# Kernel tuning notes

Hardware: AMD Instinct MI355X
Metric: run time of the kernel (lower is better)

Reference implementation:

```python
import jax, jax.numpy as jnp
import numpy as np

B, L, D, H = 2, 2048, 1024, 16
DH = D // H            # head depth = 64
LEN_CONTEXT = 2048 + 1 # module stores len_context + 1


def setup_inputs() -> dict:
    key = jax.random.key(0)
    ks = jax.random.split(key, 9)
    s = 0.02
    return {
        "query": jax.random.normal(ks[0], (B, L, D), jnp.float32),
        "key":   jax.random.normal(ks[1], (B, L, D), jnp.float32),
        "value": jax.random.normal(ks[2], (B, L, D), jnp.float32),
        "Wq": jax.random.normal(ks[3], (D, D), jnp.float32) * s,
        "bq": jnp.zeros((D,), jnp.float32),
        "Wk": jax.random.normal(ks[4], (D, D), jnp.float32) * s,
        "bk": jnp.zeros((D,), jnp.float32),
        "Wv": jax.random.normal(ks[5], (D, D), jnp.float32) * s,
        "bv": jnp.zeros((D,), jnp.float32),
        "Wo": jax.random.normal(ks[6], (D, D), jnp.float32) * s,
        "bo": jnp.zeros((D,), jnp.float32),
        "rel": jax.random.normal(ks[7], (LEN_CONTEXT, DH), jnp.float32) * s,
    }


def _split_heads(x):
    # [B, L, D] -> [B, H, L, DH]
    return x.reshape(B, L, H, DH).transpose(0, 2, 1, 3)


def reference(query, key, value, Wq, bq, Wk, bk, Wv, bv, Wo, bo, rel):
    q = _split_heads(query @ Wq + bq)   # [B,H,L,DH]
    k = _split_heads(key @ Wk + bk)
    v = _split_heads(value @ Wv + bv)

    # relative embedding slice: rel[max(0, len_context - len_q):]
    start = max(0, LEN_CONTEXT - L)
    e = rel[start:, :]                  # [M, DH], M = L here
    M = e.shape[0]

    qe = jnp.einsum('bhld,md->bhlm', q, e)  # [B,H,L,M]

    # _qe_masking: keep qe[l, m] where m >= M-1-l (upper anti-triangle)
    mask = (jnp.arange(M)[None, :] >= (M - 1 - jnp.arange(L))[:, None]).astype(qe.dtype)
    qe = qe * mask

    # _skewing: pad 1 on left of last dim, reshape swapping last two dims, drop first row
    padded = jnp.pad(qe, ((0, 0), (0, 0), (0, 0), (1, 0)))        # [B,H,L,M+1]
    reshaped = padded.reshape(B, H, M + 1, L)
    srel = reshaped[:, :, 1:, :]                                  # [B,H,L,L] (len_k == len_q)

    logits = (jnp.einsum('bhld,bhmd->bhlm', q, k) + srel) / jnp.sqrt(jnp.float32(DH))
    # NOTE: the original code builds a directional mask but never adds it to logits
    attn = jax.nn.softmax(logits, axis=-1)
    out = jnp.einsum('bhlm,bhmd->bhld', attn, v)                  # [B,H,L,DH]
    out = out.transpose(0, 2, 1, 3).reshape(B, L, D)
    return out @ Wo + bo
```

## Files before the change

### kernel.cpp

```cpp
#include <hip/hip_runtime.h>
#include <hip/hip_bf16.h>


typedef __bf16 v8bf __attribute__((ext_vector_type(8)));
typedef __bf16 v4bf __attribute__((ext_vector_type(4)));
typedef float f32x4 __attribute__((ext_vector_type(4)));
typedef float f32x16 __attribute__((ext_vector_type(16)));

#define MFMA16(A,B,C) __builtin_amdgcn_mfma_f32_16x16x32_bf16((A),(B),(C),0,0,0)
#define MFMA32(A,B,C) __builtin_amdgcn_mfma_f32_32x32x16_bf16((A),(B),(C),0,0,0)

__global__ __launch_bounds__(256)
void cast_rel(const float* __restrict__ rel, __bf16* __restrict__ E)
{
    const int i = blockIdx.x * 256 + threadIdx.x;
    if (i >= 2304 * 16) return;
    const int base = i * 4;
    const int row = base >> 6;
    const int prow = row - 128;
    v4bf o;
    if (prow >= 0 && prow < 2048) {
        const float4 v = *reinterpret_cast<const float4*>(&rel[(size_t)(prow + 1) * 64 + (base & 63)]);
        o[0] = (__bf16)v.x; o[1] = (__bf16)v.y; o[2] = (__bf16)v.z; o[3] = (__bf16)v.w;
    } else {
        o[0] = (__bf16)0.f; o[1] = (__bf16)0.f; o[2] = (__bf16)0.f; o[3] = (__bf16)0.f;
    }
    *reinterpret_cast<v4bf*>(&E[base]) = o;
}

__global__ __launch_bounds__(256)
void transpose_cast_w4(const float* __restrict__ W0, const float* __restrict__ W1,
                       const float* __restrict__ W2, const float* __restrict__ W3,
                       __bf16* __restrict__ Wt4)
{
    __shared__ float tile[64][65];
    const int z = blockIdx.z;
    const float* W = (z == 0) ? W0 : (z == 1) ? W1 : (z == 2) ? W2 : W3;
    __bf16* Wt = Wt4 + (size_t)z * 1048576;
    const int r0 = blockIdx.y * 64, c0 = blockIdx.x * 64;
    const int tr = threadIdx.x >> 4;
    const int tc = (threadIdx.x & 15) * 4;
    #pragma unroll
    for (int p = 0; p < 4; ++p) {
        const int r = tr + p * 16;
        const float4 v = *reinterpret_cast<const float4*>(&W[(size_t)(r0 + r) * 1024 + c0 + tc]);
        tile[r][tc + 0] = v.x; tile[r][tc + 1] = v.y; tile[r][tc + 2] = v.z; tile[r][tc + 3] = v.w;
    }
    __syncthreads();
    #pragma unroll
    for (int p = 0; p < 4; ++p) {
        const int cr = tr + p * 16;
        v4bf o;
        o[0] = (__bf16)tile[tc + 0][cr];
        o[1] = (__bf16)tile[tc + 1][cr];
        o[2] = (__bf16)tile[tc + 2][cr];
        o[3] = (__bf16)tile[tc + 3][cr];
        *reinterpret_cast<v4bf*>(&Wt[(size_t)(c0 + cr) * 1024 + r0 + tc]) = o;
    }
}

template <bool ABF16>
__device__ __forceinline__
void gemm_body(const float* __restrict__ Af, const __bf16* __restrict__ Ab,
               const __bf16* __restrict__ Wt, const float* __restrict__ bias,
               float* __restrict__ Cf, __bf16* __restrict__ Cb, int mode,
               int bx, int by)
{
    __shared__ __bf16 As[2][128 * 64];
    __shared__ __bf16 Ws[2][64 * 64];
    const int tid = threadIdx.x;
    const int wid = tid >> 6, lane = tid & 63, g = lane >> 4, li = lane & 15;
    const int r0 = by * 128, c0 = bx * 64;
    const int wr = wid >> 1, wc = wid & 1;
    const int sr = tid >> 3, sb = tid & 7;

    f32x4 acc[4][2];
    #pragma unroll
    for (int a = 0; a < 4; ++a)
        #pragma unroll
        for (int b2 = 0; b2 < 2; ++b2) acc[a][b2] = f32x4{0.f, 0.f, 0.f, 0.f};

    v8bf areg[4], wreg[2];

    auto loadA = [&](int p, int kt) -> v8bf {
        if constexpr (ABF16) {
            return *reinterpret_cast<const v8bf*>(&Ab[(size_t)(r0 + sr + 32 * p) * 1024 + kt + sb * 8]);
        } else {
            const float* ar = &Af[(size_t)(r0 + sr + 32 * p) * 1024 + kt + sb * 8];
            const float4 f0 = *reinterpret_cast<const float4*>(ar);
            const float4 f1 = *reinterpret_cast<const float4*>(ar + 4);
            v8bf a8;
            a8[0] = (__bf16)f0.x; a8[1] = (__bf16)f0.y; a8[2] = (__bf16)f0.z; a8[3] = (__bf16)f0.w;
            a8[4] = (__bf16)f1.x; a8[5] = (__bf16)f1.y; a8[6] = (__bf16)f1.z; a8[7] = (__bf16)f1.w;
            return a8;
        }
    };

    #pragma unroll
    for (int p = 0; p < 4; ++p) areg[p] = loadA(p, 0);
    #pragma unroll
    for (int p = 0; p < 2; ++p)
        wreg[p] = *reinterpret_cast<const v8bf*>(&Wt[(size_t)(c0 + sr + 32 * p) * 1024 + sb * 8]);
    #pragma unroll
    for (int p = 0; p < 4; ++p) {
        const int row = sr + 32 * p;
        *reinterpret_cast<v8bf*>(&As[0][row * 64 + ((sb ^ (row & 7)) << 3)]) = areg[p];
    }
    #pragma unroll
    for (int p = 0; p < 2; ++p) {
        const int row = sr + 32 * p;
        *reinterpret_cast<v8bf*>(&Ws[0][row * 64 + ((sb ^ (row & 7)) << 3)]) = wreg[p];
    }
    __syncthreads();

    for (int ki = 0; ki < 16; ++ki) {
        const int cur = ki & 1;
        if (ki < 15) {
            const int kt = (ki + 1) * 64;
            #pragma unroll
            for (int p = 0; p < 4; ++p) areg[p] = loadA(p, kt);
            #pragma unroll
            for (int p = 0; p < 2; ++p)
                wreg[p] = *reinterpret_cast<const v8bf*>(&Wt[(size_t)(c0 + sr + 32 * p) * 1024 + kt + sb * 8]);
        }
        #pragma unroll
        for (int ks = 0; ks < 2; ++ks) {
            v8bf af[4], bfr[2];
            #pragma unroll
            for (int fm = 0; fm < 4; ++fm) {
                const int row = wr * 64 + fm * 16 + li;
                af[fm] = *reinterpret_cast<const v8bf*>(
                    &As[cur][row * 64 + (((ks * 4 + g) ^ (row & 7)) << 3)]);
            }
            #pragma unroll
            for (int fn = 0; fn < 2; ++fn) {
                const int row = wc * 32 + fn * 16 + li;
                bfr[fn] = *reinterpret_cast<const v8bf*>(
                    &Ws[cur][row * 64 + (((ks * 4 + g) ^ (row & 7)) << 3)]);
            }
            __builtin_amdgcn_s_setprio(1);
            #pragma unroll
            for (int fm = 0; fm < 4; ++fm)
                #pragma unroll
                for (int fn = 0; fn < 2; ++fn)
                    acc[fm][fn] = MFMA16(af[fm], bfr[fn], acc[fm][fn]);
            __builtin_amdgcn_s_setprio(0);
        }
        if (ki < 15) {
            const int nxt = cur ^ 1;
            #pragma unroll
            for (int p = 0; p < 4; ++p) {
                const int row = sr + 32 * p;
                *reinterpret_cast<v8bf*>(&As[nxt][row * 64 + ((sb ^ (row & 7)) << 3)]) = areg[p];
            }
            #pragma unroll
            for (int p = 0; p < 2; ++p) {
                const int row = sr + 32 * p;
                *reinterpret_cast<v8bf*>(&Ws[nxt][row * 64 + ((sb ^ (row & 7)) << 3)]) = wreg[p];
            }
        }
        __syncthreads();
    }

    #pragma unroll
    for (int fn = 0; fn < 2; ++fn) {
        const int col = c0 + wc * 32 + fn * 16 + li;
        const float bb = bias[col];
        #pragma unroll
        for (int fm = 0; fm < 4; ++fm) {
            if (mode == 2) {
                const int row = r0 + wr * 64 + fm * 16 + 4 * g;
                const int b = row >> 11, l = row & 2047;
                const int h = col >> 6, dh = col & 63;
                v4bf pk;
                #pragma unroll
                for (int reg = 0; reg < 4; ++reg)
                    pk[reg] = (__bf16)(acc[fm][fn][reg] + bb);
                *reinterpret_cast<v4bf*>(&Cb[((size_t)((b * 16 + h) * 64 + dh)) * 2048 + l]) = pk;
            } else {
                #pragma unroll
                for (int reg = 0; reg < 4; ++reg) {
                    const int row = r0 + wr * 64 + fm * 16 + 4 * g + reg;
                    const float val = acc[fm][fn][reg] + bb;
                    if (mode == 0) {
                        Cf[(size_t)row * 1024 + col] = val;
                    } else {
                        const int b = row >> 11, l = row & 2047, h = col >> 6, dh = col & 63;
                        Cb[((size_t)(b * 16 + h) * 2048 + l) * 64 + dh] = (__bf16)val;
                    }
                }
            }
        }
    }
}

__global__ __launch_bounds__(256)
void gemm_proj3(const float* __restrict__ Aq, const float* __restrict__ Ak,
                const float* __restrict__ Av, const __bf16* __restrict__ Wt4,
                const float* __restrict__ bq, const float* __restrict__ bk,
                const float* __restrict__ bv, __bf16* __restrict__ qo,
                __bf16* __restrict__ ko, __bf16* __restrict__ vto)
{
    const int z = blockIdx.z;
    const float* A = (z == 0) ? Aq : (z == 1) ? Ak : Av;
    const __bf16* Wt = Wt4 + (size_t)z * 1048576;
    const float* bias = (z == 0) ? bq : (z == 1) ? bk : bv;
    __bf16* Cb = (z == 0) ? qo : (z == 1) ? ko : vto;
    gemm_body<false>(A, nullptr, Wt, bias, nullptr, Cb, (z == 2) ? 2 : 1,
                     blockIdx.x, blockIdx.y);
}

__global__ __launch_bounds__(256)
void gemm_out(const __bf16* __restrict__ A, const __bf16* __restrict__ Wt,
              const float* __restrict__ bias, float* __restrict__ C)
{
    gemm_body<true>(nullptr, A, Wt, bias, C, nullptr, 0, blockIdx.x, blockIdx.y);
}

__global__ __launch_bounds__(256, 2)
void attn_mfma(const __bf16* __restrict__ q, const __bf16* __restrict__ k,
               const __bf16* __restrict__ vt, const __bf16* __restrict__ Ep,
               __bf16* __restrict__ ao)
{
    __shared__ __bf16 Kl[64 * 64];
    __shared__ __bf16 Vl[64 * 64];
    __shared__ __bf16 Tl[4][32 * 132];
    __shared__ __bf16 Pl[4][32 * 72];

    const int tid = threadIdx.x;
    const int wid = tid >> 6;
    const int lane = tid & 63;
    const int l31 = lane & 31;
    const int g2 = lane >> 5;

    const int flat = blockIdx.y * 16 + blockIdx.x;
    const int jj_ = flat >> 3;
    const int bh = (flat & 7) * 4 + (jj_ >> 4);
    const int qt = jj_ & 15;

    const int l0 = qt * 128;
    const int lw0 = l0 + wid * 32;
    const size_t hbase = (size_t)bh * (2048 * 64);
    const __bf16* qp = q + hbase;
    const __bf16* kp = k + hbase;
    const __bf16* vtp = vt + hbase;
    const int wb0 = 1984 - l0 - 32 * wid;

    __bf16* Tw = &Tl[wid][0];
    __bf16* Pw = &Pl[wid][0];

    constexpr float kScale = 0.1803368801111244f;

    v8bf qf[4];
    {
        const __bf16* qrow = qp + (size_t)(lw0 + l31) * 64 + g2 * 8;
        qf[0] = *reinterpret_cast<const v8bf*>(qrow);
        qf[1] = *reinterpret_cast<const v8bf*>(qrow + 16);
        qf[2] = *reinterpret_cast<const v8bf*>(qrow + 32);
        qf[3] = *reinterpret_cast<const v8bf*>(qrow + 48);
    }

    const int sr = tid >> 3, sb = tid & 7;

    auto eload = [&](int baseRow, v8bf eb[8]) {
        #pragma unroll
        for (int jc = 0; jc < 2; ++jc)
            #pragma unroll
            for (int ks = 0; ks < 4; ++ks)
                eb[jc * 4 + ks] = *reinterpret_cast<const v8bf*>(
                    Ep + (size_t)(baseRow + jc * 32 + l31) * 64 + ks * 16 + g2 * 8);
    };

    auto tgemm = [&](const v8bf eb[8], int colBase) {
        #pragma unroll
        for (int jc = 0; jc < 2; ++jc) {
            f32x16 tacc;
            #pragma unroll
            for (int r = 0; r < 16; ++r) tacc[r] = 0.f;
            __builtin_amdgcn_s_setprio(1);
            #pragma unroll
            for (int ks = 0; ks < 4; ++ks)
                tacc = MFMA32(eb[jc * 4 + ks], qf[ks], tacc);
            __builtin_amdgcn_s_setprio(0);
            #pragma unroll
            for (int r2 = 0; r2 < 4; ++r2) {
                v4bf w;
                w[0] = (__bf16)tacc[4 * r2 + 0]; w[1] = (__bf16)tacc[4 * r2 + 1];
                w[2] = (__bf16)tacc[4 * r2 + 2]; w[3] = (__bf16)tacc[4 * r2 + 3];
                const int col = colBase + jc * 32 + 8 * r2 + 4 * g2;
                *reinterpret_cast<v4bf*>(Tw + l31 * 132 + col) = w;
            }
        }
    };

    {
        const v8bf k0a = *reinterpret_cast<const v8bf*>(kp + (size_t)sr * 64 + sb * 8);
        const v8bf k0b = *reinterpret_cast<const v8bf*>(kp + (size_t)(sr + 32) * 64 + sb * 8);
        const v8bf v0a = *reinterpret_cast<const v8bf*>(vtp + (size_t)sr * 2048 + sb * 8);
        const v8bf v0b = *reinterpret_cast<const v8bf*>(vtp + (size_t)(sr + 32) * 2048 + sb * 8);
        v8bf ebA[8], ebB[8];
        eload(wb0, ebA);
        eload(wb0 + 64, ebB);
        *reinterpret_cast<v8bf*>(&Kl[sr * 64 + ((sb ^ (sr & 7)) << 3)]) = k0a;
        *reinterpret_cast<v8bf*>(&Kl[(sr + 32) * 64 + ((sb ^ (sr & 7)) << 3)]) = k0b;
        *reinterpret_cast<v8bf*>(&Vl[sr * 64 + ((sb ^ (sr & 7)) << 3)]) = v0a;
        *reinterpret_cast<v8bf*>(&Vl[(sr + 32) * 64 + ((sb ^ (sr & 7)) << 3)]) = v0b;
        __syncthreads();
        tgemm(ebA, 0);
        tgemm(ebB, 64);
    }

    f32x16 oacc[2];
    #pragma unroll
    for (int dc = 0; dc < 2; ++dc)
        #pragma unroll
        for (int r = 0; r < 16; ++r) oacc[dc][r] = 0.f;
    float lrow = 0.f;

    for (int t = 0; t < 32; ++t) {
        const int m0 = t * 64;
        const bool lastT = (t == 31);
        const bool needRel = (m0 <= lw0 + 31);
        const bool fullAdd = (m0 + 63 <= lw0);
        const bool needTnext = (m0 + 64 <= lw0 + 31);
        const int lob = 64 * (t & 1);

        v8bf ebN[8];
        if (needTnext) eload(wb0 + 64 * t + 128, ebN);

        v8bf kra, krb, vra, vrb;
        if (!lastT) {
            const int m1 = m0 + 64;
            kra = *reinterpret_cast<const v8bf*>(kp + (size_t)(m1 + sr) * 64 + sb * 8);
            krb = *reinterpret_cast<const v8bf*>(kp + (size_t)(m1 + sr + 32) * 64 + sb * 8);
            vra = *reinterpret_cast<const v8bf*>(vtp + (size_t)sr * 2048 + m1 + sb * 8);
            vrb = *reinterpret_cast<const v8bf*>(vtp + (size_t)(sr + 32) * 2048 + m1 + sb * 8);
        }

        #pragma unroll
        for (int mc = 0; mc < 2; ++mc) {
            f32x16 sacc;
            #pragma unroll
            for (int r = 0; r < 16; ++r) sacc[r] = 0.f;
            __builtin_amdgcn_s_setprio(1);
            #pragma unroll
            for (int ks = 0; ks < 4; ++ks) {
                const int row = mc * 32 + l31;
                const v8bf kb = *reinterpret_cast<const v8bf*>(
                    &Kl[row * 64 + (((2 * ks + g2) ^ (l31 & 7)) << 3)]);
                sacc = MFMA32(kb, qf[ks], sacc);
            }
            __builtin_amdgcn_s_setprio(0);

            if (needRel) {
                const int cb = 63 - l31 + lob;
                if (fullAdd) {
                    #pragma unroll
                    for (int r2 = 0; r2 < 4; ++r2)
                        #pragma unroll
                        for (int i2 = 0; i2 < 4; ++i2) {
                            const int mtl = mc * 32 + 8 * r2 + 4 * g2 + i2;
                            const int c = (cb + mtl) & 127;
                            sacc[4 * r2 + i2] += (float)Tw[l31 * 132 + c];
                        }
                } else {
                    const int R = lw0 + l31 - m0;
                    #pragma unroll
                    for (int r2 = 0; r2 < 4; ++r2)
                        #pragma unroll
                        for (int i2 = 0; i2 < 4; ++i2) {
                            const int mtl = mc * 32 + 8 * r2 + 4 * g2 + i2;
                            const int c = (cb + mtl) & 127;
                            const float tv = (float)Tw[l31 * 132 + c];
                            sacc[4 * r2 + i2] += (mtl <= R) ? tv : 0.f;
                        }
                }
            }

            #pragma unroll
            for (int jj = 0; jj < 4; ++jj) {
                const float p0 = exp2f(sacc[4 * jj + 0] * kScale);
                const float p1 = exp2f(sacc[4 * jj + 1] * kScale);
                const float p2 = exp2f(sacc[4 * jj + 2] * kScale);
                const float p3 = exp2f(sacc[4 * jj + 3] * kScale);
                lrow += (p0 + p1) + (p2 + p3);
                v4bf w;
                w[0] = (__bf16)p0; w[1] = (__bf16)p1; w[2] = (__bf16)p2; w[3] = (__bf16)p3;
                *reinterpret_cast<v4bf*>(Pw + l31 * 72 + mc * 32 + 8 * jj + 4 * g2) = w;
            }
        }

        if (needTnext) tgemm(ebN, lob);

        #pragma unroll
        for (int ks = 0; ks < 4; ++ks) {
            const v8bf pa = *reinterpret_cast<const v8bf*>(Pw + l31 * 72 + ks * 16 + g2 * 8);
            __builtin_amdgcn_s_setprio(1);
            #pragma unroll
            for (int dc = 0; dc < 2; ++dc) {
                const int row = dc * 32 + l31;
                const v8bf vb = *reinterpret_cast<const v8bf*>(
                    &Vl[row * 64 + (((2 * ks + g2) ^ (l31 & 7)) << 3)]);
                oacc[dc] = MFMA32(vb, pa, oacc[dc]);
            }
            __builtin_amdgcn_s_setprio(0);
        }

        __syncthreads();
        if (!lastT) {
            *reinterpret_cast<v8bf*>(&Kl[sr * 64 + ((sb ^ (sr & 7)) << 3)]) = kra;
            *reinterpret_cast<v8bf*>(&Kl[(sr + 32) * 64 + ((sb ^ (sr & 7)) << 3)]) = krb;
            *reinterpret_cast<v8bf*>(&Vl[sr * 64 + ((sb ^ (sr & 7)) << 3)]) = vra;
            *reinterpret_cast<v8bf*>(&Vl[(sr + 32) * 64 + ((sb ^ (sr & 7)) << 3)]) = vrb;
        }
        __syncthreads();
    }

    lrow += __shfl_xor(lrow, 32);
    const float inv = 1.0f / lrow;

    __syncthreads();
    __bf16* Ol = &Tl[0][0];
    #pragma unroll
    for (int dc = 0; dc < 2; ++dc)
        #pragma unroll
        for (int r2 = 0; r2 < 4; ++r2) {
            v4bf w;
            w[0] = (__bf16)(oacc[dc][4 * r2 + 0] * inv);
            w[1] = (__bf16)(oacc[dc][4 * r2 + 1] * inv);
            w[2] = (__bf16)(oacc[dc][4 * r2 + 2] * inv);
            w[3] = (__bf16)(oacc[dc][4 * r2 + 3] * inv);
            const int d0 = dc * 32 + 8 * r2 + 4 * g2;
            *reinterpret_cast<v4bf*>(Ol + (wid * 32 + l31) * 72 + d0) = w;
        }
    __syncthreads();

    const int b = bh >> 4, h = bh & 15;
    #pragma unroll
    for (int p = 0; p < 4; ++p) {
        const int row = p * 32 + (tid >> 3);
        const v8bf w = *reinterpret_cast<const v8bf*>(Ol + row * 72 + (tid & 7) * 8);
        *reinterpret_cast<v8bf*>(ao + (size_t)(b * 2048 + l0 + row) * 1024 + h * 64 + (tid & 7) * 8) = w;
    }
}

extern "C" void kernel_launch(void* const* d_in, const int* in_sizes, int n_in,
                              void* d_out, int out_size, void* d_ws, size_t ws_size,
                              hipStream_t stream) {
    (void)in_sizes; (void)n_in; (void)out_size; (void)ws_size;
    const float* query = (const float*)d_in[0];
    const float* key   = (const float*)d_in[1];
    const float* value = (const float*)d_in[2];
    const float* Wq    = (const float*)d_in[3];
    const float* bq    = (const float*)d_in[4];
    const float* Wk    = (const float*)d_in[5];
    const float* bk    = (const float*)d_in[6];
    const float* Wv    = (const float*)d_in[7];
    const float* bv    = (const float*)d_in[8];
    const float* Wo    = (const float*)d_in[9];
    const float* bo    = (const float*)d_in[10];
    const float* rel   = (const float*)d_in[11];
    float* out = (float*)d_out;

    __bf16* q_bf  = (__bf16*)d_ws;
    __bf16* k_bf  = q_bf + 4194304;
    __bf16* vt_bf = k_bf + 4194304;
    __bf16* Wt4   = vt_bf + 4194304;
    __bf16* E_pad = Wt4 + 4194304;
    __bf16* aob   = E_pad + 147456;

    const dim3 blk(256);

    cast_rel<<<144, blk, 0, stream>>>(rel, E_pad);
    transpose_cast_w4<<<dim3(16, 16, 4), blk, 0, stream>>>(Wq, Wk, Wv, Wo, Wt4);
    gemm_proj3<<<dim3(16, 32, 3), blk, 0, stream>>>(query, key, value, Wt4,
                                                    bq, bk, bv, q_bf, k_bf, vt_bf);
    attn_mfma<<<dim3(16, 32), blk, 0, stream>>>(q_bf, k_bf, vt_bf, E_pad + 128 * 64, aob);
    gemm_out<<<dim3(16, 32), blk, 0, stream>>>(aob, Wt4 + 3 * 1048576, bo, out);
}
```

Measured before the change: 203.5 us.

## Split attention into single-wave blocks loading K/V directly from global

The attention kernel changes from 256-thread blocks that share K/V tiles in LDS to 64-thread single-wave blocks, each handling 32 query rows. Each wave loads K and V fragments straight from global/L2 into registers, which removes the LDS staging and all __syncthreads barriers. The softmax scale (which includes the log2 factor) is now folded into the Q projection epilogue, so the per-element multiply before exp2 goes away. In exchange, global K/V traffic rises roughly fourfold, since the four waves no longer share tiles, and more vector registers are held live per wave.

```diff
diff --git a/kernel.cpp b/kernel.cpp
--- a/kernel.cpp
+++ b/kernel.cpp
@@ -9,6 +9,8 @@
 
 #define MFMA16(A,B,C) __builtin_amdgcn_mfma_f32_16x16x32_bf16((A),(B),(C),0,0,0)
 #define MFMA32(A,B,C) __builtin_amdgcn_mfma_f32_32x32x16_bf16((A),(B),(C),0,0,0)
+
+constexpr float kQScale = 0.1803368801111244f;
 
 __global__ __launch_bounds__(256)
 void cast_rel(const float* __restrict__ rel, __bf16* __restrict__ E)
@@ -64,7 +66,7 @@
 void gemm_body(const float* __restrict__ Af, const __bf16* __restrict__ Ab,
                const __bf16* __restrict__ Wt, const float* __restrict__ bias,
                float* __restrict__ Cf, __bf16* __restrict__ Cb, int mode,
-               int bx, int by)
+               float oscale, int bx, int by)
 {
     __shared__ __bf16 As[2][128 * 64];
     __shared__ __bf16 Ws[2][64 * 64];
@@ -186,7 +188,7 @@
                         Cf[(size_t)row * 1024 + col] = val;
                     } else {
                         const int b = row >> 11, l = row & 2047, h = col >> 6, dh = col & 63;
-                        Cb[((size_t)(b * 16 + h) * 2048 + l) * 64 + dh] = (__bf16)val;
+                        Cb[((size_t)(b * 16 + h) * 2048 + l) * 64 + dh] = (__bf16)(val * oscale);
                     }
                 }
             }
@@ -206,7 +208,8 @@
     const __bf16* Wt = Wt4 + (size_t)z * 1048576;
     const float* bias = (z == 0) ? bq : (z == 1) ? bk : bv;
     __bf16* Cb = (z == 0) ? qo : (z == 1) ? ko : vto;
-    gemm_body<false>(A, nullptr, Wt, bias, nullptr, Cb, (z == 2) ? 2 : 1,
+    const float osc = (z == 0) ? kQScale : 1.0f;
+    gemm_body<false>(A, nullptr, Wt, bias, nullptr, Cb, (z == 2) ? 2 : 1, osc,
                      blockIdx.x, blockIdx.y);
 }
 
@@ -214,42 +217,32 @@
 void gemm_out(const __bf16* __restrict__ A, const __bf16* __restrict__ Wt,
               const float* __restrict__ bias, float* __restrict__ C)
 {
-    gemm_body<true>(nullptr, A, Wt, bias, C, nullptr, 0, blockIdx.x, blockIdx.y);
-}
-
-__global__ __launch_bounds__(256, 2)
+    gemm_body<true>(nullptr, A, Wt, bias, C, nullptr, 0, 1.0f, blockIdx.x, blockIdx.y);
+}
+
+__global__ __launch_bounds__(64)
 void attn_mfma(const __bf16* __restrict__ q, const __bf16* __restrict__ k,
                const __bf16* __restrict__ vt, const __bf16* __restrict__ Ep,
                __bf16* __restrict__ ao)
 {
-    __shared__ __bf16 Kl[64 * 64];
-    __shared__ __bf16 Vl[64 * 64];
-    __shared__ __bf16 Tl[4][32 * 132];
-    __shared__ __bf16 Pl[4][32 * 72];
+    __shared__ __bf16 Tw[32 * 132];
+    __shared__ __bf16 Pw[32 * 72];
 
     const int tid = threadIdx.x;
-    const int wid = tid >> 6;
-    const int lane = tid & 63;
-    const int l31 = lane & 31;
-    const int g2 = lane >> 5;
-
-    const int flat = blockIdx.y * 16 + blockIdx.x;
-    const int jj_ = flat >> 3;
-    const int bh = (flat & 7) * 4 + (jj_ >> 4);
-    const int qt = jj_ & 15;
-
-    const int l0 = qt * 128;
-    const int lw0 = l0 + wid * 32;
+    const int l31 = tid & 31;
+    const int g2 = tid >> 5;
+
+    const int flat = blockIdx.x;
+    const int xcd = flat & 7;
+    const int idx = flat >> 3;
+    const int bh = xcd * 4 + (idx >> 6);
+    const int lw0 = (idx & 63) * 32;
+
     const size_t hbase = (size_t)bh * (2048 * 64);
     const __bf16* qp = q + hbase;
     const __bf16* kp = k + hbase;
     const __bf16* vtp = vt + hbase;
-    const int wb0 = 1984 - l0 - 32 * wid;
-
-    __bf16* Tw = &Tl[wid][0];
-    __bf16* Pw = &Pl[wid][0];
-
-    constexpr float kScale = 0.1803368801111244f;
+    const int wb0 = 1984 - lw0;
 
     v8bf qf[4];
     {
@@ -260,15 +253,13 @@
         qf[3] = *reinterpret_cast<const v8bf*>(qrow + 48);
     }
 
-    const int sr = tid >> 3, sb = tid & 7;
-
     auto eload = [&](int baseRow, v8bf eb[8]) {
         #pragma unroll
         for (int jc = 0; jc < 2; ++jc)
             #pragma unroll
             for (int ks = 0; ks < 4; ++ks)
                 eb[jc * 4 + ks] = *reinterpret_cast<const v8bf*>(
-                    Ep + (size_t)(baseRow + jc * 32 + l31) * 64 + ks * 16 + g2 * 8);
+                    Ep + (long)(baseRow + jc * 32 + l31) * 64 + ks * 16 + g2 * 8);
     };
 
     auto tgemm = [&](const v8bf eb[8], int colBase) {
@@ -287,25 +278,16 @@
                 v4bf w;
                 w[0] = (__bf16)tacc[4 * r2 + 0]; w[1] = (__bf16)tacc[4 * r2 + 1];
                 w[2] = (__bf16)tacc[4 * r2 + 2]; w[3] = (__bf16)tacc[4 * r2 + 3];
-                const int col = colBase + jc * 32 + 8 * r2 + 4 * g2;
-                *reinterpret_cast<v4bf*>(Tw + l31 * 132 + col) = w;
+                *reinterpret_cast<v4bf*>(
+                    &Tw[l31 * 132 + colBase + jc * 32 + 8 * r2 + 4 * g2]) = w;
             }
         }
     };
 
     {
-        const v8bf k0a = *reinterpret_cast<const v8bf*>(kp + (size_t)sr * 64 + sb * 8);
-        const v8bf k0b = *reinterpret_cast<const v8bf*>(kp + (size_t)(sr + 32) * 64 + sb * 8);
-        const v8bf v0a = *reinterpret_cast<const v8bf*>(vtp + (size_t)sr * 2048 + sb * 8);
-        const v8bf v0b = *reinterpret_cast<const v8bf*>(vtp + (size_t)(sr + 32) * 2048 + sb * 8);
         v8bf ebA[8], ebB[8];
         eload(wb0, ebA);
         eload(wb0 + 64, ebB);
-        *reinterpret_cast<v8bf*>(&Kl[sr * 64 + ((sb ^ (sr & 7)) << 3)]) = k0a;
-        *reinterpret_cast<v8bf*>(&Kl[(sr + 32) * 64 + ((sb ^ (sr & 7)) << 3)]) = k0b;
-        *reinterpret_cast<v8bf*>(&Vl[sr * 64 + ((sb ^ (sr & 7)) << 3)]) = v0a;
-        *reinterpret_cast<v8bf*>(&Vl[(sr + 32) * 64 + ((sb ^ (sr & 7)) << 3)]) = v0b;
-        __syncthreads();
         tgemm(ebA, 0);
         tgemm(ebB, 64);
     }
@@ -319,37 +301,38 @@
 
     for (int t = 0; t < 32; ++t) {
         const int m0 = t * 64;
-        const bool lastT = (t == 31);
         const bool needRel = (m0 <= lw0 + 31);
         const bool fullAdd = (m0 + 63 <= lw0);
         const bool needTnext = (m0 + 64 <= lw0 + 31);
         const int lob = 64 * (t & 1);
 
         v8bf ebN[8];
-        if (needTnext) eload(wb0 + 64 * t + 128, ebN);
-
-        v8bf kra, krb, vra, vrb;
-        if (!lastT) {
-            const int m1 = m0 + 64;
-            kra = *reinterpret_cast<const v8bf*>(kp + (size_t)(m1 + sr) * 64 + sb * 8);
-            krb = *reinterpret_cast<const v8bf*>(kp + (size_t)(m1 + sr + 32) * 64 + sb * 8);
-            vra = *reinterpret_cast<const v8bf*>(vtp + (size_t)sr * 2048 + m1 + sb * 8);
-            vrb = *reinterpret_cast<const v8bf*>(vtp + (size_t)(sr + 32) * 2048 + m1 + sb * 8);
+        if (needTnext) eload(wb0 + m0 + 128, ebN);
+
+        v8bf vb0[4], vb1[4];
+        #pragma unroll
+        for (int ks = 0; ks < 4; ++ks) {
+            vb0[ks] = *reinterpret_cast<const v8bf*>(
+                vtp + (size_t)(l31) * 2048 + m0 + ks * 16 + g2 * 8);
+            vb1[ks] = *reinterpret_cast<const v8bf*>(
+                vtp + (size_t)(32 + l31) * 2048 + m0 + ks * 16 + g2 * 8);
         }
 
         #pragma unroll
         for (int mc = 0; mc < 2; ++mc) {
+            v8bf kb[4];
+            #pragma unroll
+            for (int ks = 0; ks < 4; ++ks)
+                kb[ks] = *reinterpret_cast<const v8bf*>(
+                    kp + (size_t)(m0 + mc * 32 + l31) * 64 + ks * 16 + g2 * 8);
+
             f32x16 sacc;
             #pragma unroll
             for (int r = 0; r < 16; ++r) sacc[r] = 0.f;
             __builtin_amdgcn_s_setprio(1);
             #pragma unroll
-            for (int ks = 0; ks < 4; ++ks) {
-                const int row = mc * 32 + l31;
-                const v8bf kb = *reinterpret_cast<const v8bf*>(
-                    &Kl[row * 64 + (((2 * ks + g2) ^ (l31 & 7)) << 3)]);
-                sacc = MFMA32(kb, qf[ks], sacc);
-            }
+            for (int ks = 0; ks < 4; ++ks)
+                sacc = MFMA32(kb[ks], qf[ks], sacc);
             __builtin_amdgcn_s_setprio(0);
 
             if (needRel) {
@@ -378,15 +361,15 @@
             }
 
             #pragma unroll
-            for (int jj = 0; jj < 4; ++jj) {
-                const float p0 = exp2f(sacc[4 * jj + 0] * kScale);
-                const float p1 = exp2f(sacc[4 * jj + 1] * kScale);
-                const float p2 = exp2f(sacc[4 * jj + 2] * kScale);
-                const float p3 = exp2f(sacc[4 * jj + 3] * kScale);
+            for (int r2 = 0; r2 < 4; ++r2) {
+                const float p0 = exp2f(sacc[4 * r2 + 0]);
+                const float p1 = exp2f(sacc[4 * r2 + 1]);
+                const float p2 = exp2f(sacc[4 * r2 + 2]);
+                const float p3 = exp2f(sacc[4 * r2 + 3]);
                 lrow += (p0 + p1) + (p2 + p3);
                 v4bf w;
                 w[0] = (__bf16)p0; w[1] = (__bf16)p1; w[2] = (__bf16)p2; w[3] = (__bf16)p3;
-                *reinterpret_cast<v4bf*>(Pw + l31 * 72 + mc * 32 + 8 * jj + 4 * g2) = w;
+                *reinterpret_cast<v4bf*>(&Pw[l31 * 72 + mc * 32 + 8 * r2 + 4 * g2]) = w;
             }
         }
 
@@ -394,53 +377,35 @@
 
         #pragma unroll
         for (int ks = 0; ks < 4; ++ks) {
-            const v8bf pa = *reinterpret_cast<const v8bf*>(Pw + l31 * 72 + ks * 16 + g2 * 8);
+            const v8bf pf = *reinterpret_cast<const v8bf*>(&Pw[l31 * 72 + ks * 16 + g2 * 8]);
             __builtin_amdgcn_s_setprio(1);
-            #pragma unroll
-            for (int dc = 0; dc < 2; ++dc) {
-                const int row = dc * 32 + l31;
-                const v8bf vb = *reinterpret_cast<const v8bf*>(
-                    &Vl[row * 64 + (((2 * ks + g2) ^ (l31 & 7)) << 3)]);
-                oacc[dc] = MFMA32(vb, pa, oacc[dc]);
-            }
+            oacc[0] = MFMA32(vb0[ks], pf, oacc[0]);
+            oacc[1] = MFMA32(vb1[ks], pf, oacc[1]);
             __builtin_amdgcn_s_setprio(0);
         }
-
-        __syncthreads();
-        if (!lastT) {
-            *reinterpret_cast<v8bf*>(&Kl[sr * 64 + ((sb ^ (sr & 7)) << 3)]) = kra;
-            *reinterpret_cast<v8bf*>(&Kl[(sr + 32) * 64 + ((sb ^ (sr & 7)) << 3)]) = krb;
-            *reinterpret_cast<v8bf*>(&Vl[sr * 64 + ((sb ^ (sr & 7)) << 3)]) = vra;
-            *reinterpret_cast<v8bf*>(&Vl[(sr + 32) * 64 + ((sb ^ (sr & 7)) << 3)]) = vrb;
-        }
-        __syncthreads();
     }
 
     lrow += __shfl_xor(lrow, 32);
     const float inv = 1.0f / lrow;
 
-    __syncthreads();
-    __bf16* Ol = &Tl[0][0];
     #pragma unroll
     for (int dc = 0; dc < 2; ++dc)
         #pragma unroll
         for (int r2 = 0; r2 < 4; ++r2) {
-            v4bf w;
-            w[0] = (__bf16)(oacc[dc][4 * r2 + 0] * inv);
-            w[1] = (__bf16)(oacc[dc][4 * r2 + 1] * inv);
-            w[2] = (__bf16)(oacc[dc][4 * r2 + 2] * inv);
-            w[3] = (__bf16)(oacc[dc][4 * r2 + 3] * inv);
-            const int d0 = dc * 32 + 8 * r2 + 4 * g2;
-            *reinterpret_cast<v4bf*>(Ol + (wid * 32 + l31) * 72 + d0) = w;
-        }
-    __syncthreads();
-
+            v4bf wv;
+            wv[0] = (__bf16)(oacc[dc][4 * r2 + 0] * inv);
+            wv[1] = (__bf16)(oacc[dc][4 * r2 + 1] * inv);
+            wv[2] = (__bf16)(oacc[dc][4 * r2 + 2] * inv);
+            wv[3] = (__bf16)(oacc[dc][4 * r2 + 3] * inv);
+            *reinterpret_cast<v4bf*>(&Tw[l31 * 72 + dc * 32 + 8 * r2 + 4 * g2]) = wv;
+        }
     const int b = bh >> 4, h = bh & 15;
+    const int row = tid >> 1, ch = tid & 1;
     #pragma unroll
     for (int p = 0; p < 4; ++p) {
-        const int row = p * 32 + (tid >> 3);
-        const v8bf w = *reinterpret_cast<const v8bf*>(Ol + row * 72 + (tid & 7) * 8);
-        *reinterpret_cast<v8bf*>(ao + (size_t)(b * 2048 + l0 + row) * 1024 + h * 64 + (tid & 7) * 8) = w;
+        const v8bf o8 = *reinterpret_cast<const v8bf*>(&Tw[row * 72 + ch * 32 + p * 8]);
+        *reinterpret_cast<v8bf*>(
+            ao + (size_t)(b * 2048 + lw0 + row) * 1024 + h * 64 + ch * 32 + p * 8) = o8;
     }
 }
 
@@ -475,6 +440,7 @@
     transpose_cast_w4<<<dim3(16, 16, 4), blk, 0, stream>>>(Wq, Wk, Wv, Wo, Wt4);
     gemm_proj3<<<dim3(16, 32, 3), blk, 0, stream>>>(query, key, value, Wt4,
                                                     bq, bk, bv, q_bf, k_bf, vt_bf);
-    attn_mfma<<<dim3(16, 32), blk, 0, stream>>>(q_bf, k_bf, vt_bf, E_pad + 128 * 64, aob);
+    attn_mfma<<<dim3(2048), dim3(64), 0, stream>>>(q_bf, k_bf, vt_bf,
+                                                   E_pad + 128 * 64, aob);
     gemm_out<<<dim3(16, 32), blk, 0, stream>>>(aob, Wt4 + 3 * 1048576, bo, out);
 }
```

Result: slower. 261.3 us (+28.4%).
